# Kernel tuning notes

Hardware: AMD Instinct MI355X
Metric: run time of the kernel (lower is better)

Reference implementation:

```python
import jax, jax.numpy as jnp
import numpy as np

N_NODES = 50000
N_EDGES = 500000
IN_DIM = 128
HIDDEN = 32
HEADS = 8
OUT_DIM = HIDDEN * HEADS  # 256
NEG_SLOPE = 0.2


def setup_inputs() -> dict:
    key = jax.random.key(0)
    ks = jax.random.split(key, 10)
    s = lambda fan: 1.0 / np.sqrt(fan)
    x = jax.random.normal(ks[0], (N_NODES, IN_DIM), dtype=jnp.float32)
    edge_index = jax.random.randint(ks[1], (2, N_EDGES), 0, N_NODES, dtype=jnp.int32)
    W1 = jax.random.normal(ks[2], (IN_DIM, HEADS * HIDDEN), jnp.float32) * s(IN_DIM)
    a_src1 = jax.random.normal(ks[3], (HEADS, HIDDEN), jnp.float32) * s(HIDDEN)
    a_dst1 = jax.random.normal(ks[4], (HEADS, HIDDEN), jnp.float32) * s(HIDDEN)
    b1 = jnp.zeros((HEADS * HIDDEN,), jnp.float32)
    W2 = jax.random.normal(ks[5], (OUT_DIM, OUT_DIM), jnp.float32) * s(OUT_DIM)
    a_src2 = jax.random.normal(ks[6], (1, OUT_DIM), jnp.float32) * s(OUT_DIM)
    a_dst2 = jax.random.normal(ks[7], (1, OUT_DIM), jnp.float32) * s(OUT_DIM)
    b2 = jnp.zeros((OUT_DIM,), jnp.float32)
    return {"x": x, "edge_index": edge_index, "W1": W1, "a_src1": a_src1,
            "a_dst1": a_dst1, "b1": b1, "W2": W2, "a_src2": a_src2,
            "a_dst2": a_dst2, "b2": b2}


def _gat_layer(x, src, dst, W, a_src, a_dst, b, heads, ch, concat):
    N = x.shape[0]
    h = (x @ W).reshape(N, heads, ch)                      # [N,H,C]
    e_src = jnp.sum(h * a_src[None], axis=-1)              # [N,H]
    e_dst = jnp.sum(h * a_dst[None], axis=-1)              # [N,H]
    e = jax.nn.leaky_relu(e_src[src] + e_dst[dst], NEG_SLOPE)  # [E,H]
    # softmax over incoming edges of each destination node
    m = jax.ops.segment_max(e, dst, num_segments=N)        # [N,H]
    e = jnp.exp(e - m[dst])
    denom = jax.ops.segment_sum(e, dst, num_segments=N)    # [N,H]
    alpha = e / (denom[dst] + 1e-16)                       # [E,H]
    msg = h[src] * alpha[:, :, None]                       # [E,H,C]
    out = jax.ops.segment_sum(msg, dst, num_segments=N)    # [N,H,C]
    out = out.reshape(N, heads * ch) if concat else out.mean(axis=1)
    return out + b


def reference(x, edge_index, W1, a_src1, a_dst1, b1, W2, a_src2, a_dst2, b2):
    N = x.shape[0]
    # add self loops (PyG GATConv default)
    loops = jnp.arange(N, dtype=edge_index.dtype)
    src = jnp.concatenate([edge_index[0], loops])
    dst = jnp.concatenate([edge_index[1], loops])
    # dropout is identity in eval mode
    h = _gat_layer(x, src, dst, W1, a_src1, a_dst1, b1, HEADS, HIDDEN, True)
    h = jax.nn.elu(h)
    out = _gat_layer(h, src, dst, W2, a_src2, a_dst2, b2, 1, OUT_DIM, False)
    return out
```

## Files before the change

kernel.cpp:

```cpp
#include <hip/hip_runtime.h>
#include <math.h>

#define N_NODES 50000
#define E_ORIG  500000
#define E_TOT   550000
#define NB      196

typedef _Float16 half8 __attribute__((ext_vector_type(8)));
typedef _Float16 half4 __attribute__((ext_vector_type(4)));
typedef float    v4f   __attribute__((ext_vector_type(4)));

__global__ void k_zero(int* __restrict__ p, int n) {
    int i = blockIdx.x * blockDim.x + threadIdx.x;
    if (i < n) p[i] = 0;
}

__global__ void k_count(const int* __restrict__ ei, int* __restrict__ deg) {
    int e = blockIdx.x * blockDim.x + threadIdx.x;
    if (e >= E_TOT) return;
    int d = (e < E_ORIG) ? ei[E_ORIG + e] : (e - E_ORIG);
    atomicAdd(&deg[d], 1);
}

__global__ __launch_bounds__(256) void k_blocksum(const int* __restrict__ deg,
                                                  int* __restrict__ bsum) {
    int t = threadIdx.x;
    int i = blockIdx.x * 256 + t;
    int v = (i < N_NODES) ? deg[i] : 0;
#pragma unroll
    for (int mk = 1; mk < 64; mk <<= 1) v += __shfl_xor(v, mk, 64);
    __shared__ int ws[4];
    if ((t & 63) == 0) ws[t >> 6] = v;
    __syncthreads();
    if (t == 0) bsum[blockIdx.x] = ws[0] + ws[1] + ws[2] + ws[3];
}

__global__ __launch_bounds__(256) void k_scanbsum(const int* __restrict__ bsum,
                                                  int* __restrict__ boff) {
    __shared__ int s[256];
    int t = threadIdx.x;
    int v = (t < NB) ? bsum[t] : 0;
    s[t] = v;
    __syncthreads();
    for (int o = 1; o < 256; o <<= 1) {
        int x = (t >= o) ? s[t - o] : 0;
        __syncthreads();
        s[t] += x;
        __syncthreads();
    }
    if (t <= NB) boff[t] = (t == 0) ? 0 : s[t - 1];
}

__global__ __launch_bounds__(256) void k_offsets(const int* __restrict__ deg,
                                                 const int* __restrict__ boff,
                                                 int* __restrict__ offsets,
                                                 int* __restrict__ cur) {
    __shared__ int s[256];
    int t = threadIdx.x;
    int i = blockIdx.x * 256 + t;
    int v = (i < N_NODES) ? deg[i] : 0;
    s[t] = v;
    __syncthreads();
    for (int o = 1; o < 256; o <<= 1) {
        int x = (t >= o) ? s[t - o] : 0;
        __syncthreads();
        s[t] += x;
        __syncthreads();
    }
    int off = boff[blockIdx.x] + s[t] - v;
    if (i <= N_NODES) {
        offsets[i] = off;
        if (i < N_NODES) cur[i] = off;
    }
}

__global__ void k_scatter(const int* __restrict__ ei, int* __restrict__ cur,
                          int* __restrict__ csr_src) {
    int e = blockIdx.x * blockDim.x + threadIdx.x;
    if (e >= E_TOT) return;
    int s, d;
    if (e < E_ORIG) { s = ei[e]; d = ei[E_ORIG + e]; }
    else            { s = e - E_ORIG; d = s; }
    int slot = atomicAdd(&cur[d], 1);
    csr_src[slot] = s;
}

#define N4X (N_NODES * 128 / 4)
__global__ void k_prep(const float* __restrict__ X, _Float16* __restrict__ Xh,
                       const float* __restrict__ W1, _Float16* __restrict__ w1t,
                       const float* __restrict__ W2, _Float16* __restrict__ w2t) {
    int i = blockIdx.x * blockDim.x + threadIdx.x;
    if (i < N4X) {
        float4 v = ((const float4*)X)[i];
        ((half4*)Xh)[i] = (half4){(_Float16)v.x, (_Float16)v.y, (_Float16)v.z, (_Float16)v.w};
        return;
    }
    int j = i - N4X;
    if (j < 128 * 256) {
        int k = j >> 8, c = j & 255;
        w1t[(size_t)c * 128 + k] = (_Float16)W1[j];
        return;
    }
    j -= 128 * 256;
    if (j < 256 * 256) {
        int k = j >> 8, c = j & 255;
        w2t[(size_t)c * 256 + k] = (_Float16)W2[j];
    }
}

__global__ __launch_bounds__(256) void k_vw2(const float* __restrict__ W2,
                                             const float* __restrict__ as2,
                                             const float* __restrict__ ad2,
                                             float* __restrict__ vs2,
                                             float* __restrict__ vd2) {
    int k = threadIdx.x;
    float s = 0.f, d = 0.f;
    for (int c = 0; c < 256; c++) {
        float w = W2[(size_t)k * 256 + c];
        s += w * as2[c];
        d += w * ad2[c];
    }
    vs2[k] = s;
    vd2[k] = d;
}

__global__ __launch_bounds__(256) void k_gemm1(
    const _Float16* __restrict__ A, const _Float16* __restrict__ Bt,
    const float* __restrict__ a_s, const float* __restrict__ a_d,
    _Float16* __restrict__ H, float* __restrict__ es, float* __restrict__ ed) {
    constexpr int K = 128;
    int t = threadIdx.x, w = t >> 6, lane = t & 63;
    int quad = lane >> 4, l16 = lane & 15;
    int rh = w & 1, ch = w >> 1;
    int row0 = blockIdx.x * 64 + rh * 32;
    int colbase = ch * 128;

    v4f acc[2][8];
#pragma unroll
    for (int i = 0; i < 2; i++)
#pragma unroll
        for (int j = 0; j < 8; j++) acc[i][j] = (v4f){0.f, 0.f, 0.f, 0.f};

    int r0 = row0 + l16;      if (r0 >= N_NODES) r0 = N_NODES - 1;
    int r1 = row0 + 16 + l16; if (r1 >= N_NODES) r1 = N_NODES - 1;
    const half8* a0 = (const half8*)(A + (size_t)r0 * K + quad * 8);
    const half8* a1 = (const half8*)(A + (size_t)r1 * K + quad * 8);
    const half8* bp[8];
#pragma unroll
    for (int ct = 0; ct < 8; ct++)
        bp[ct] = (const half8*)(Bt + (size_t)(colbase + ct * 16 + l16) * K + quad * 8);

#pragma unroll
    for (int kc = 0; kc < K / 32; kc++) {
        half8 av0 = a0[kc * 4];
        half8 av1 = a1[kc * 4];
#pragma unroll
        for (int ct = 0; ct < 8; ct++) {
            half8 bv = bp[ct][kc * 4];
            acc[0][ct] = __builtin_amdgcn_mfma_f32_16x16x32_f16(av0, bv, acc[0][ct], 0, 0, 0);
            acc[1][ct] = __builtin_amdgcn_mfma_f32_16x16x32_f16(av1, bv, acc[1][ct], 0, 0, 0);
        }
    }

#pragma unroll
    for (int rt = 0; rt < 2; rt++) {
#pragma unroll
        for (int reg = 0; reg < 4; reg++) {
            int row = row0 + rt * 16 + quad * 4 + reg;
            if (row < N_NODES) {
#pragma unroll
                for (int ct = 0; ct < 8; ct++)
                    H[(size_t)row * 256 + colbase + ct * 16 + l16] = (_Float16)acc[rt][ct][reg];
            }
        }
    }

    float asv[8], adv[8];
#pragma unroll
    for (int ct = 0; ct < 8; ct++) {
        asv[ct] = a_s[colbase + ct * 16 + l16];
        adv[ct] = a_d[colbase + ct * 16 + l16];
    }

#pragma unroll
    for (int rt = 0; rt < 2; rt++) {
#pragma unroll
        for (int hp = 0; hp < 4; hp++) {
#pragma unroll
            for (int reg = 0; reg < 4; reg++) {
                float ps = acc[rt][2 * hp][reg] * asv[2 * hp] +
                           acc[rt][2 * hp + 1][reg] * asv[2 * hp + 1];
                float pd = acc[rt][2 * hp][reg] * adv[2 * hp] +
                           acc[rt][2 * hp + 1][reg] * adv[2 * hp + 1];
#pragma unroll
                for (int mk = 1; mk < 16; mk <<= 1) {
                    ps += __shfl_xor(ps, mk, 64);
                    pd += __shfl_xor(pd, mk, 64);
                }
                if (l16 == 0) {
                    int row = row0 + rt * 16 + quad * 4 + reg;
                    if (row < N_NODES) {
                        int head = ch * 4 + hp;
                        es[(size_t)row * 8 + head] = ps;
                        ed[(size_t)row * 8 + head] = pd;
                    }
                }
            }
        }
    }
}

__global__ __launch_bounds__(256) void k_gemm2(
    const _Float16* __restrict__ A, const _Float16* __restrict__ Bt,
    const float* __restrict__ bias, float* __restrict__ OUT) {
    constexpr int K = 256;
    int t = threadIdx.x, w = t >> 6, lane = t & 63;
    int quad = lane >> 4, l16 = lane & 15;
    int rh = w & 1, ch = w >> 1;
    int row0 = blockIdx.x * 64 + rh * 32;
    int colbase = ch * 128;

    v4f acc[2][8];
#pragma unroll
    for (int i = 0; i < 2; i++)
#pragma unroll
        for (int j = 0; j < 8; j++) acc[i][j] = (v4f){0.f, 0.f, 0.f, 0.f};

    int r0 = row0 + l16;      if (r0 >= N_NODES) r0 = N_NODES - 1;
    int r1 = row0 + 16 + l16; if (r1 >= N_NODES) r1 = N_NODES - 1;
    const half8* a0 = (const half8*)(A + (size_t)r0 * K + quad * 8);
    const half8* a1 = (const half8*)(A + (size_t)r1 * K + quad * 8);
    const half8* bp[8];
#pragma unroll
    for (int ct = 0; ct < 8; ct++)
        bp[ct] = (const half8*)(Bt + (size_t)(colbase + ct * 16 + l16) * K + quad * 8);

#pragma unroll
    for (int kc = 0; kc < K / 32; kc++) {
        half8 av0 = a0[kc * 4];
        half8 av1 = a1[kc * 4];
#pragma unroll
        for (int ct = 0; ct < 8; ct++) {
            half8 bv = bp[ct][kc * 4];
            acc[0][ct] = __builtin_amdgcn_mfma_f32_16x16x32_f16(av0, bv, acc[0][ct], 0, 0, 0);
            acc[1][ct] = __builtin_amdgcn_mfma_f32_16x16x32_f16(av1, bv, acc[1][ct], 0, 0, 0);
        }
    }

    float bv[8];
#pragma unroll
    for (int ct = 0; ct < 8; ct++) bv[ct] = bias[colbase + ct * 16 + l16];

#pragma unroll
    for (int rt = 0; rt < 2; rt++) {
#pragma unroll
        for (int reg = 0; reg < 4; reg++) {
            int row = row0 + rt * 16 + quad * 4 + reg;
            if (row < N_NODES) {
#pragma unroll
                for (int ct = 0; ct < 8; ct++)
                    OUT[(size_t)row * 256 + colbase + ct * 16 + l16] =
                        acc[rt][ct][reg] + bv[ct];
            }
        }
    }
}

__global__ __launch_bounds__(256) void k_agg1(
    const _Float16* __restrict__ H1, const float* __restrict__ es,
    const float* __restrict__ ed, const int* __restrict__ offsets,
    const int* __restrict__ csr_src, const float* __restrict__ b1,
    const float* __restrict__ vs2, const float* __restrict__ vd2,
    _Float16* __restrict__ out1, float* __restrict__ es2,
    float* __restrict__ ed2) {
    int t = threadIdx.x, w = t >> 6, lane = t & 63;
    int n = blockIdx.x * 4 + w;
    int hB = lane >> 3;
    int beg = offsets[n];
    int deg = offsets[n + 1] - beg;
    float edl = ed[(size_t)n * 8 + hB];

    const half4* __restrict__ Hl = (const half4*)H1 + lane;
    float a0 = 0.f, a1 = 0.f, a2 = 0.f, a3 = 0.f, den = 0.f;

    for (int base = 0; base < deg; base += 64) {
        int rem = deg - base; if (rem > 64) rem = 64;
        int idx = beg + base + lane;
        if (idx >= E_TOT) idx = E_TOT - 1;
        int sreg = csr_src[idx];
        int i = 0;
        for (; i + 1 < rem; i += 2) {
            int s0 = __shfl(sreg, i);
            int s1 = __shfl(sreg, i + 1);
            float l0 = es[(size_t)s0 * 8 + hB] + edl;
            float l1 = es[(size_t)s1 * 8 + hB] + edl;
            l0 = l0 > 0.f ? l0 : 0.2f * l0;
            l1 = l1 > 0.f ? l1 : 0.2f * l1;
            float w0 = __expf(l0), w1 = __expf(l1);
            half4 h0 = Hl[(size_t)s0 * 64];
            half4 h1 = Hl[(size_t)s1 * 64];
            a0 += w0 * (float)h0[0]; a1 += w0 * (float)h0[1];
            a2 += w0 * (float)h0[2]; a3 += w0 * (float)h0[3];
            a0 += w1 * (float)h1[0]; a1 += w1 * (float)h1[1];
            a2 += w1 * (float)h1[2]; a3 += w1 * (float)h1[3];
            den += w0 + w1;
        }
        if (i < rem) {
            int s0 = __shfl(sreg, i);
            float l0 = es[(size_t)s0 * 8 + hB] + edl;
            l0 = l0 > 0.f ? l0 : 0.2f * l0;
            float w0 = __expf(l0);
            half4 h0 = Hl[(size_t)s0 * 64];
            a0 += w0 * (float)h0[0]; a1 += w0 * (float)h0[1];
            a2 += w0 * (float)h0[2]; a3 += w0 * (float)h0[3];
            den += w0;
        }
    }

    float r = 1.f / (den + 1e-16f);
    float4 bb = ((const float4*)b1)[lane];
    float o0 = a0 * r + bb.x, o1 = a1 * r + bb.y;
    float o2 = a2 * r + bb.z, o3 = a3 * r + bb.w;
    o0 = o0 > 0.f ? o0 : __expf(o0) - 1.f;
    o1 = o1 > 0.f ? o1 : __expf(o1) - 1.f;
    o2 = o2 > 0.f ? o2 : __expf(o2) - 1.f;
    o3 = o3 > 0.f ? o3 : __expf(o3) - 1.f;
    ((half4*)(out1 + (size_t)n * 256))[lane] =
        (half4){(_Float16)o0, (_Float16)o1, (_Float16)o2, (_Float16)o3};

    float4 vs = ((const float4*)vs2)[lane];
    float4 vd = ((const float4*)vd2)[lane];
    float ps = o0 * vs.x + o1 * vs.y + o2 * vs.z + o3 * vs.w;
    float pd = o0 * vd.x + o1 * vd.y + o2 * vd.z + o3 * vd.w;
#pragma unroll
    for (int mk = 1; mk < 64; mk <<= 1) {
        ps += __shfl_xor(ps, mk, 64);
        pd += __shfl_xor(pd, mk, 64);
    }
    if (lane == 0) { es2[n] = ps; ed2[n] = pd; }
}

__global__ __launch_bounds__(256) void k_agg2(
    const _Float16* __restrict__ O1, const float* __restrict__ es2,
    const float* __restrict__ ed2, const int* __restrict__ offsets,
    const int* __restrict__ csr_src, _Float16* __restrict__ xagg) {
    int t = threadIdx.x, w = t >> 6, lane = t & 63;
    int n = blockIdx.x * 4 + w;
    int beg = offsets[n];
    int deg = offsets[n + 1] - beg;
    float edn = ed2[n];

    const half4* __restrict__ Ol = (const half4*)O1 + lane;
    float a0 = 0.f, a1 = 0.f, a2 = 0.f, a3 = 0.f, den = 0.f;

    for (int base = 0; base < deg; base += 64) {
        int rem = deg - base; if (rem > 64) rem = 64;
        int idx = beg + base + lane;
        if (idx >= E_TOT) idx = E_TOT - 1;
        int sreg = csr_src[idx];
        int i = 0;
        for (; i + 1 < rem; i += 2) {
            int s0 = __shfl(sreg, i);
            int s1 = __shfl(sreg, i + 1);
            float l0 = es2[s0] + edn;
            float l1 = es2[s1] + edn;
            l0 = l0 > 0.f ? l0 : 0.2f * l0;
            l1 = l1 > 0.f ? l1 : 0.2f * l1;
            float w0 = __expf(l0), w1 = __expf(l1);
            half4 h0 = Ol[(size_t)s0 * 64];
            half4 h1 = Ol[(size_t)s1 * 64];
            a0 += w0 * (float)h0[0]; a1 += w0 * (float)h0[1];
            a2 += w0 * (float)h0[2]; a3 += w0 * (float)h0[3];
            a0 += w1 * (float)h1[0]; a1 += w1 * (float)h1[1];
            a2 += w1 * (float)h1[2]; a3 += w1 * (float)h1[3];
            den += w0 + w1;
        }
        if (i < rem) {
            int s0 = __shfl(sreg, i);
            float l0 = es2[s0] + edn;
            l0 = l0 > 0.f ? l0 : 0.2f * l0;
            float w0 = __expf(l0);
            half4 h0 = Ol[(size_t)s0 * 64];
            a0 += w0 * (float)h0[0]; a1 += w0 * (float)h0[1];
            a2 += w0 * (float)h0[2]; a3 += w0 * (float)h0[3];
            den += w0;
        }
    }

    float r = 1.f / (den + 1e-16f);
    ((half4*)(xagg + (size_t)n * 256))[lane] =
        (half4){(_Float16)(a0 * r), (_Float16)(a1 * r),
                (_Float16)(a2 * r), (_Float16)(a3 * r)};
}

extern "C" void kernel_launch(void* const* d_in, const int* in_sizes, int n_in,
                              void* d_out, int out_size, void* d_ws, size_t ws_size,
                              hipStream_t stream) {
    const float* x   = (const float*)d_in[0];
    const int*   ei  = (const int*)d_in[1];
    const float* W1  = (const float*)d_in[2];
    const float* as1 = (const float*)d_in[3];
    const float* ad1 = (const float*)d_in[4];
    const float* b1  = (const float*)d_in[5];
    const float* W2  = (const float*)d_in[6];
    const float* as2 = (const float*)d_in[7];
    const float* ad2 = (const float*)d_in[8];
    const float* b2  = (const float*)d_in[9];
    float* out = (float*)d_out;

    char* ws = (char*)d_ws;
    size_t off = 0;
    auto alloc = [&](size_t bytes) {
        void* p = ws + off;
        off = (off + bytes + 255) & ~(size_t)255;
        return p;
    };
    _Float16* h1h     = (_Float16*)alloc((size_t)N_NODES * 256 * 2);
    _Float16* out1h   = (_Float16*)alloc((size_t)N_NODES * 256 * 2);
    _Float16* xagg    = (_Float16*)alloc((size_t)N_NODES * 256 * 2);
    _Float16* xh      = (_Float16*)alloc((size_t)N_NODES * 128 * 2);
    _Float16* w1t     = (_Float16*)alloc((size_t)128 * 256 * 2);
    _Float16* w2t     = (_Float16*)alloc((size_t)256 * 256 * 2);
    float*    es1     = (float*)alloc((size_t)N_NODES * 8 * 4);
    float*    ed1     = (float*)alloc((size_t)N_NODES * 8 * 4);
    float*    es2     = (float*)alloc((size_t)N_NODES * 4);
    float*    ed2     = (float*)alloc((size_t)N_NODES * 4);
    float*    vs2     = (float*)alloc(256 * 4);
    float*    vd2     = (float*)alloc(256 * 4);
    int*      deg     = (int*)alloc((size_t)N_NODES * 4);
    int*      offsets = (int*)alloc((size_t)(N_NODES + 1) * 4);
    int*      cur     = (int*)alloc((size_t)N_NODES * 4);
    int*      csr_src = (int*)alloc((size_t)E_TOT * 4);
    int*      bsum    = (int*)alloc((size_t)NB * 4);
    int*      boff    = (int*)alloc((size_t)(NB + 1) * 4);

    const int TB = 256;
    int gridN = (N_NODES + TB - 1) / TB;
    int gridE = (E_TOT + TB - 1) / TB;
    int gridG = (N_NODES + 63) / 64;
    int gridA = N_NODES / 4;

    k_zero<<<gridN, TB, 0, stream>>>(deg, N_NODES);
    k_count<<<gridE, TB, 0, stream>>>(ei, deg);
    k_blocksum<<<NB, TB, 0, stream>>>(deg, bsum);
    k_scanbsum<<<1, TB, 0, stream>>>(bsum, boff);
    k_offsets<<<NB, TB, 0, stream>>>(deg, boff, offsets, cur);
    k_scatter<<<gridE, TB, 0, stream>>>(ei, cur, csr_src);

    int prepN = N4X + 128 * 256 + 256 * 256;
    k_prep<<<(prepN + TB - 1) / TB, TB, 0, stream>>>(x, xh, W1, w1t, W2, w2t);
    k_vw2<<<1, TB, 0, stream>>>(W2, as2, ad2, vs2, vd2);

    k_gemm1<<<gridG, TB, 0, stream>>>(xh, w1t, as1, ad1, h1h, es1, ed1);
    k_agg1<<<gridA, TB, 0, stream>>>(h1h, es1, ed1, offsets, csr_src, b1,
                                     vs2, vd2, out1h, es2, ed2);

    k_agg2<<<gridA, TB, 0, stream>>>(out1h, es2, ed2, offsets, csr_src, xagg);
    k_gemm2<<<gridG, TB, 0, stream>>>(xagg, w2t, b2, out);
}
```

Before: 340.6 us.

## Fuse X fp16 conversion into GEMM1, merge prep kernels, stage GEMM outputs via LDS

GEMM1 now reads fp32 X directly and converts it to fp16 in registers. This removes the separate X conversion pass and the Xh buffer round trip. The weight-prep and vw2 kernels are merged into one launch. Both GEMMs switch to 32-row blocks with each wave owning 64 columns, and they stage results through shared memory so global stores become coalesced 16-byte writes. The cost is that GEMM1 reads twice the bytes for X, plus extra LDS traffic and a barrier.

```diff
diff --git a/kernel.cpp b/kernel.cpp
--- a/kernel.cpp
+++ b/kernel.cpp
@@ -85,107 +85,85 @@
     csr_src[slot] = s;
 }
 
-#define N4X (N_NODES * 128 / 4)
-__global__ void k_prep(const float* __restrict__ X, _Float16* __restrict__ Xh,
-                       const float* __restrict__ W1, _Float16* __restrict__ w1t,
-                       const float* __restrict__ W2, _Float16* __restrict__ w2t) {
+__global__ void k_prepw(const float* __restrict__ W1, const float* __restrict__ W2,
+                        const float* __restrict__ as2, const float* __restrict__ ad2,
+                        _Float16* __restrict__ w1t, _Float16* __restrict__ w2t,
+                        float* __restrict__ vs2, float* __restrict__ vd2) {
     int i = blockIdx.x * blockDim.x + threadIdx.x;
-    if (i < N4X) {
-        float4 v = ((const float4*)X)[i];
-        ((half4*)Xh)[i] = (half4){(_Float16)v.x, (_Float16)v.y, (_Float16)v.z, (_Float16)v.w};
+    if (i < 128 * 256) {
+        int k = i >> 8, c = i & 255;
+        w1t[(size_t)c * 128 + k] = (_Float16)W1[i];
         return;
     }
-    int j = i - N4X;
-    if (j < 128 * 256) {
-        int k = j >> 8, c = j & 255;
-        w1t[(size_t)c * 128 + k] = (_Float16)W1[j];
-        return;
-    }
-    j -= 128 * 256;
+    int j = i - 128 * 256;
     if (j < 256 * 256) {
         int k = j >> 8, c = j & 255;
         w2t[(size_t)c * 256 + k] = (_Float16)W2[j];
-    }
-}
-
-__global__ __launch_bounds__(256) void k_vw2(const float* __restrict__ W2,
-                                             const float* __restrict__ as2,
-                                             const float* __restrict__ ad2,
-                                             float* __restrict__ vs2,
-                                             float* __restrict__ vd2) {
-    int k = threadIdx.x;
-    float s = 0.f, d = 0.f;
-    for (int c = 0; c < 256; c++) {
-        float w = W2[(size_t)k * 256 + c];
-        s += w * as2[c];
-        d += w * ad2[c];
-    }
-    vs2[k] = s;
-    vd2[k] = d;
+        return;
+    }
+    int k = j - 256 * 256;
+    if (k < 256) {
+        float s = 0.f, d = 0.f;
+        for (int c = 0; c < 256; c++) {
+            float w = W2[(size_t)k * 256 + c];
+            s += w * as2[c];
+            d += w * ad2[c];
+        }
+        vs2[k] = s;
+        vd2[k] = d;
+    }
 }
 
 __global__ __launch_bounds__(256) void k_gemm1(
-    const _Float16* __restrict__ A, const _Float16* __restrict__ Bt,
+    const float* __restrict__ X, const _Float16* __restrict__ Bt,
     const float* __restrict__ a_s, const float* __restrict__ a_d,
     _Float16* __restrict__ H, float* __restrict__ es, float* __restrict__ ed) {
-    constexpr int K = 128;
     int t = threadIdx.x, w = t >> 6, lane = t & 63;
     int quad = lane >> 4, l16 = lane & 15;
-    int rh = w & 1, ch = w >> 1;
-    int row0 = blockIdx.x * 64 + rh * 32;
-    int colbase = ch * 128;
-
-    v4f acc[2][8];
+    int row0 = blockIdx.x * 32;
+    int colbase = w * 64;
+
+    v4f acc[2][4];
 #pragma unroll
     for (int i = 0; i < 2; i++)
 #pragma unroll
-        for (int j = 0; j < 8; j++) acc[i][j] = (v4f){0.f, 0.f, 0.f, 0.f};
+        for (int j = 0; j < 4; j++) acc[i][j] = (v4f){0.f, 0.f, 0.f, 0.f};
 
     int r0 = row0 + l16;      if (r0 >= N_NODES) r0 = N_NODES - 1;
     int r1 = row0 + 16 + l16; if (r1 >= N_NODES) r1 = N_NODES - 1;
-    const half8* a0 = (const half8*)(A + (size_t)r0 * K + quad * 8);
-    const half8* a1 = (const half8*)(A + (size_t)r1 * K + quad * 8);
-    const half8* bp[8];
-#pragma unroll
-    for (int ct = 0; ct < 8; ct++)
-        bp[ct] = (const half8*)(Bt + (size_t)(colbase + ct * 16 + l16) * K + quad * 8);
-
-#pragma unroll
-    for (int kc = 0; kc < K / 32; kc++) {
-        half8 av0 = a0[kc * 4];
-        half8 av1 = a1[kc * 4];
-#pragma unroll
-        for (int ct = 0; ct < 8; ct++) {
+    const float4* a0p = (const float4*)(X + (size_t)r0 * 128) + quad * 2;
+    const float4* a1p = (const float4*)(X + (size_t)r1 * 128) + quad * 2;
+    const half8* bp[4];
+#pragma unroll
+    for (int ct = 0; ct < 4; ct++)
+        bp[ct] = (const half8*)(Bt + (size_t)(colbase + ct * 16 + l16) * 128 + quad * 8);
+
+#pragma unroll
+    for (int kc = 0; kc < 4; kc++) {
+        float4 f0 = a0p[kc * 8], f1 = a0p[kc * 8 + 1];
+        float4 f2 = a1p[kc * 8], f3 = a1p[kc * 8 + 1];
+        half8 av0 = (half8){(_Float16)f0.x, (_Float16)f0.y, (_Float16)f0.z, (_Float16)f0.w,
+                            (_Float16)f1.x, (_Float16)f1.y, (_Float16)f1.z, (_Float16)f1.w};
+        half8 av1 = (half8){(_Float16)f2.x, (_Float16)f2.y, (_Float16)f2.z, (_Float16)f2.w,
+                            (_Float16)f3.x, (_Float16)f3.y, (_Float16)f3.z, (_Float16)f3.w};
+#pragma unroll
+        for (int ct = 0; ct < 4; ct++) {
             half8 bv = bp[ct][kc * 4];
             acc[0][ct] = __builtin_amdgcn_mfma_f32_16x16x32_f16(av0, bv, acc[0][ct], 0, 0, 0);
             acc[1][ct] = __builtin_amdgcn_mfma_f32_16x16x32_f16(av1, bv, acc[1][ct], 0, 0, 0);
         }
     }
 
-#pragma unroll
-    for (int rt = 0; rt < 2; rt++) {
-#pragma unroll
-        for (int reg = 0; reg < 4; reg++) {
-            int row = row0 + rt * 16 + quad * 4 + reg;
-            if (row < N_NODES) {
-#pragma unroll
-                for (int ct = 0; ct < 8; ct++)
-                    H[(size_t)row * 256 + colbase + ct * 16 + l16] = (_Float16)acc[rt][ct][reg];
-            }
-        }
-    }
-
-    float asv[8], adv[8];
-#pragma unroll
-    for (int ct = 0; ct < 8; ct++) {
+    float asv[4], adv[4];
+#pragma unroll
+    for (int ct = 0; ct < 4; ct++) {
         asv[ct] = a_s[colbase + ct * 16 + l16];
         adv[ct] = a_d[colbase + ct * 16 + l16];
     }
-
 #pragma unroll
     for (int rt = 0; rt < 2; rt++) {
 #pragma unroll
-        for (int hp = 0; hp < 4; hp++) {
+        for (int hp = 0; hp < 2; hp++) {
 #pragma unroll
             for (int reg = 0; reg < 4; reg++) {
                 float ps = acc[rt][2 * hp][reg] * asv[2 * hp] +
@@ -200,7 +178,7 @@
                 if (l16 == 0) {
                     int row = row0 + rt * 16 + quad * 4 + reg;
                     if (row < N_NODES) {
-                        int head = ch * 4 + hp;
+                        int head = w * 2 + hp;
                         es[(size_t)row * 8 + head] = ps;
                         ed[(size_t)row * 8 + head] = pd;
                     }
@@ -208,60 +186,81 @@
             }
         }
     }
+
+    __shared__ _Float16 SH[32][264];
+#pragma unroll
+    for (int rt = 0; rt < 2; rt++)
+#pragma unroll
+        for (int ct = 0; ct < 4; ct++)
+#pragma unroll
+            for (int reg = 0; reg < 4; reg++)
+                SH[rt * 16 + quad * 4 + reg][colbase + ct * 16 + l16] =
+                    (_Float16)acc[rt][ct][reg];
+    __syncthreads();
+#pragma unroll
+    for (int j = 0; j < 4; j++) {
+        int c = j * 256 + t;
+        int row = c >> 5, col8 = c & 31;
+        int gr = row0 + row;
+        if (gr < N_NODES)
+            *(half8*)(H + (size_t)gr * 256 + col8 * 8) = *(const half8*)&SH[row][col8 * 8];
+    }
 }
 
 __global__ __launch_bounds__(256) void k_gemm2(
     const _Float16* __restrict__ A, const _Float16* __restrict__ Bt,
     const float* __restrict__ bias, float* __restrict__ OUT) {
-    constexpr int K = 256;
     int t = threadIdx.x, w = t >> 6, lane = t & 63;
     int quad = lane >> 4, l16 = lane & 15;
-    int rh = w & 1, ch = w >> 1;
-    int row0 = blockIdx.x * 64 + rh * 32;
-    int colbase = ch * 128;
-
-    v4f acc[2][8];
+    int row0 = blockIdx.x * 32;
+    int colbase = w * 64;
+
+    v4f acc[2][4];
 #pragma unroll
     for (int i = 0; i < 2; i++)
 #pragma unroll
-        for (int j = 0; j < 8; j++) acc[i][j] = (v4f){0.f, 0.f, 0.f, 0.f};
+        for (int j = 0; j < 4; j++) acc[i][j] = (v4f){0.f, 0.f, 0.f, 0.f};
 
     int r0 = row0 + l16;      if (r0 >= N_NODES) r0 = N_NODES - 1;
     int r1 = row0 + 16 + l16; if (r1 >= N_NODES) r1 = N_NODES - 1;
-    const half8* a0 = (const half8*)(A + (size_t)r0 * K + quad * 8);
-    const half8* a1 = (const half8*)(A + (size_t)r1 * K + quad * 8);
-    const half8* bp[8];
-#pragma unroll
-    for (int ct = 0; ct < 8; ct++)
-        bp[ct] = (const half8*)(Bt + (size_t)(colbase + ct * 16 + l16) * K + quad * 8);
-
-#pragma unroll
-    for (int kc = 0; kc < K / 32; kc++) {
+    const half8* a0 = (const half8*)(A + (size_t)r0 * 256 + quad * 8);
+    const half8* a1 = (const half8*)(A + (size_t)r1 * 256 + quad * 8);
+    const half8* bp[4];
+#pragma unroll
+    for (int ct = 0; ct < 4; ct++)
+        bp[ct] = (const half8*)(Bt + (size_t)(colbase + ct * 16 + l16) * 256 + quad * 8);
+
+#pragma unroll
+    for (int kc = 0; kc < 8; kc++) {
         half8 av0 = a0[kc * 4];
         half8 av1 = a1[kc * 4];
 #pragma unroll
-        for (int ct = 0; ct < 8; ct++) {
+        for (int ct = 0; ct < 4; ct++) {
             half8 bv = bp[ct][kc * 4];
             acc[0][ct] = __builtin_amdgcn_mfma_f32_16x16x32_f16(av0, bv, acc[0][ct], 0, 0, 0);
             acc[1][ct] = __builtin_amdgcn_mfma_f32_16x16x32_f16(av1, bv, acc[1][ct], 0, 0, 0);
         }
     }
 
-    float bv[8];
-#pragma unroll
-    for (int ct = 0; ct < 8; ct++) bv[ct] = bias[colbase + ct * 16 + l16];
-
-#pragma unroll
-    for (int rt = 0; rt < 2; rt++) {
-#pragma unroll
-        for (int reg = 0; reg < 4; reg++) {
-            int row = row0 + rt * 16 + quad * 4 + reg;
-            if (row < N_NODES) {
-#pragma unroll
-                for (int ct = 0; ct < 8; ct++)
-                    OUT[(size_t)row * 256 + colbase + ct * 16 + l16] =
-                        acc[rt][ct][reg] + bv[ct];
-            }
+    __shared__ float SF[32][260];
+#pragma unroll
+    for (int rt = 0; rt < 2; rt++)
+#pragma unroll
+        for (int ct = 0; ct < 4; ct++)
+#pragma unroll
+            for (int reg = 0; reg < 4; reg++)
+                SF[rt * 16 + quad * 4 + reg][colbase + ct * 16 + l16] = acc[rt][ct][reg];
+    __syncthreads();
+#pragma unroll
+    for (int j = 0; j < 8; j++) {
+        int c = j * 256 + t;
+        int row = c >> 6, c4 = c & 63;
+        int gr = row0 + row;
+        if (gr < N_NODES) {
+            float4 v = *(const float4*)&SF[row][c4 * 4];
+            float4 bb = ((const float4*)bias)[c4];
+            float4 o = make_float4(v.x + bb.x, v.y + bb.y, v.z + bb.z, v.w + bb.w);
+            *(float4*)(OUT + (size_t)gr * 256 + c4 * 4) = o;
         }
     }
 }
@@ -418,7 +417,6 @@
     _Float16* h1h     = (_Float16*)alloc((size_t)N_NODES * 256 * 2);
     _Float16* out1h   = (_Float16*)alloc((size_t)N_NODES * 256 * 2);
     _Float16* xagg    = (_Float16*)alloc((size_t)N_NODES * 256 * 2);
-    _Float16* xh      = (_Float16*)alloc((size_t)N_NODES * 128 * 2);
     _Float16* w1t     = (_Float16*)alloc((size_t)128 * 256 * 2);
     _Float16* w2t     = (_Float16*)alloc((size_t)256 * 256 * 2);
     float*    es1     = (float*)alloc((size_t)N_NODES * 8 * 4);
@@ -437,7 +435,7 @@
     const int TB = 256;
     int gridN = (N_NODES + TB - 1) / TB;
     int gridE = (E_TOT + TB - 1) / TB;
-    int gridG = (N_NODES + 63) / 64;
+    int gridG = (N_NODES + 31) / 32;
     int gridA = N_NODES / 4;
 
     k_zero<<<gridN, TB, 0, stream>>>(deg, N_NODES);
@@ -447,11 +445,11 @@
     k_offsets<<<NB, TB, 0, stream>>>(deg, boff, offsets, cur);
     k_scatter<<<gridE, TB, 0, stream>>>(ei, cur, csr_src);
 
-    int prepN = N4X + 128 * 256 + 256 * 256;
-    k_prep<<<(prepN + TB - 1) / TB, TB, 0, stream>>>(x, xh, W1, w1t, W2, w2t);
-    k_vw2<<<1, TB, 0, stream>>>(W2, as2, ad2, vs2, vd2);
-
-    k_gemm1<<<gridG, TB, 0, stream>>>(xh, w1t, as1, ad1, h1h, es1, ed1);
+    int prepN = 128 * 256 + 256 * 256 + 256;
+    k_prepw<<<(prepN + TB - 1) / TB, TB, 0, stream>>>(W1, W2, as2, ad2,
+                                                      w1t, w2t, vs2, vd2);
+
+    k_gemm1<<<gridG, TB, 0, stream>>>(x, w1t, as1, ad1, h1h, es1, ed1);
     k_agg1<<<gridA, TB, 0, stream>>>(h1h, es1, ed1, offsets, csr_src, b1,
                                      vs2, vd2, out1h, es2, ed2);
 
```

Result: faster. 329.0 us (-3.4%).
